# Optimization experiments

Measured on AMD Instinct MI355X. Metric: run time of the kernel, lower is better.

Reference implementation:

```python
import jax, jax.numpy as jnp
import numpy as np

T, B, C = 512, 64, 512
ALPHA = 0.6        # blend coefficient from __init__
TAU = 10.0         # LIF tau
VTH = 1.0          # LIF v_threshold (v_reset = 0, hard reset)
BN_EPS = 1e-5


def spike_fn(x):
    # forward heaviside: spike = (v - v_th >= 0)
    return (x >= 0.0).astype(x.dtype)


def setup_inputs() -> dict:
    key = jax.random.key(0)
    ks = jax.random.split(key, 7)
    x = jax.random.normal(ks[0], (T, B, C), dtype=jnp.float32)
    conv_w = jax.random.normal(ks[1], (C, C, 3), dtype=jnp.float32) / np.sqrt(3.0 * C)
    conv_b = jax.random.normal(ks[2], (C,), dtype=jnp.float32) * 0.01
    bn_gamma = 0.5 + jax.random.uniform(ks[3], (C,), dtype=jnp.float32)
    bn_beta = jax.random.normal(ks[4], (C,), dtype=jnp.float32) * 0.1
    bn_mean = jax.random.normal(ks[5], (C,), dtype=jnp.float32) * 0.1
    bn_var = 0.5 + jax.random.uniform(ks[6], (C,), dtype=jnp.float32)
    return {"x": x, "conv_w": conv_w, "conv_b": conv_b,
            "bn_gamma": bn_gamma, "bn_beta": bn_beta,
            "bn_mean": bn_mean, "bn_var": bn_var}


def reference(x, conv_w, conv_b, bn_gamma, bn_beta, bn_mean, bn_var):
    # x: (T, B, C). Conv1d(k=3, pad=1) on a length-1 sequence reduces to a
    # dense matmul with the middle kernel tap: out = prev @ w[:,:,1].T + b.
    w1 = conv_w[:, :, 1]                      # (C_out, C_in)
    inv_std = bn_gamma * jax.lax.rsqrt(bn_var + BN_EPS)   # fused BN scale
    Bsz, Csz = x.shape[1], x.shape[2]

    def step(carry, x_t):
        prev, v = carry                        # prev: (B, C), v: (B, C) membrane
        conv = jnp.einsum('bc,dc->bd', prev, w1) + conv_b
        bn = (conv - bn_mean) * inv_std + bn_beta
        # LIF (decay_input=True, v_reset=0): v += (x - v) / tau
        v = v + (bn - v) / TAU
        s = spike_fn(v - VTH)
        v = v * (1.0 - s)                      # hard reset to 0
        new = (1.0 - ALPHA) * x_t + ALPHA * s  # alpha blend
        return (new, v), new                   # prev_state detached in torch; no-op for fwd

    init = (jnp.zeros((Bsz, Csz), x.dtype), jnp.zeros((Bsz, Csz), x.dtype))
    _, out = jax.lax.scan(step, init, x)       # out: (T, B, C)
    return out
```

## Files before the change

kernel.cpp:

```cpp
#include <hip/hip_runtime.h>
#include <hip/hip_bf16.h>
#include <stdint.h>

#define T_STEPS 512
#define BATCH 64
#define CH 512

using short8 = __attribute__((ext_vector_type(8))) short;
using f32x4  = __attribute__((ext_vector_type(4))) float;

__device__ __forceinline__ unsigned short f2b(float f) {
    union { __hip_bfloat16 h; unsigned short u; } c;
    c.h = __float2bfloat16(f);
    return c.u;
}
__device__ __forceinline__ float b2f(unsigned short h) {
    union { unsigned u; float f; } c; c.u = ((unsigned)h) << 16;
    return c.f;
}

#define LDS_BARRIER() do {                                   \
    __builtin_amdgcn_sched_barrier(0);                       \
    asm volatile("s_waitcnt lgkmcnt(0)" ::: "memory");       \
    __builtin_amdgcn_s_barrier();                            \
    __builtin_amdgcn_sched_barrier(0);                       \
} while (0)

__global__ void prep(const float* __restrict__ cw, const float* __restrict__ cb,
                     const float* __restrict__ gamma, const float* __restrict__ beta,
                     const float* __restrict__ mean, const float* __restrict__ var,
                     unsigned short* __restrict__ wb,
                     float* __restrict__ wt,
                     float* __restrict__ isb,
                     float* __restrict__ k0p,
                     int* __restrict__ flag) {
    int idx = blockIdx.x * 256 + threadIdx.x;
    if (idx == 0) *flag = 0x7fffffff;
    if (idx >= CH * CH) return;
    int d = idx >> 9, c = idx & 511;
    float is = gamma[d] * rsqrtf(var[d] + 1e-5f);
    float w = cw[((size_t)d * CH + c) * 3 + 1];
    wb[idx] = f2b(0.04f * is * w);
    wt[(size_t)c * CH + d] = w;
    if (c == 0) {
        isb[d] = is;
        k0p[d] = 0.1f * ((cb[d] - mean[d]) * is + beta[d]);
    }
}

#define GBM 128
#define PADK 40

__global__ __launch_bounds__(512, 2) void gemm_fused(
    const float* __restrict__ Xp,
    const unsigned short* __restrict__ wbp,
    const float* __restrict__ k0p,
    unsigned short* __restrict__ Wbuf,
    float* __restrict__ outp,
    int Mc)
{
    __shared__ __align__(16) unsigned short As[2][GBM][PADK];
    __shared__ __align__(16) unsigned short Bs[2][512][PADK];
    int tid = threadIdx.x;
    int lane = tid & 63, wid = tid >> 6;
    int wm = wid >> 2, wn = wid & 3;
    int i0 = blockIdx.x * GBM;
    int fm = lane & 15, fq = lane >> 4;
    int kq = fq * 8;

    int ar = tid >> 2;
    int ak = (tid & 3) * 8;

    int grow = i0 + ar;
    bool arv = grow < Mc;
    int growc = arv ? grow : (Mc - 1);
    const float* xrow = &Xp[(size_t)growc * CH + ak];
    float* orow = &outp[(size_t)grow * CH + ak];
    const unsigned short* brow = &wbp[(size_t)ar * CH + ak];

    f32x4 acc[4][8] = {};

    float4 sa0[2], sa1[2];
    short8 sb[2][4];

    {
        sa0[0] = *(const float4*)&xrow[0];
        sa1[0] = *(const float4*)&xrow[4];
        #pragma unroll
        for (int p = 0; p < 4; ++p)
            sb[0][p] = *(const short8*)&brow[(size_t)p * 128 * CH];
        short8 av;
        av[0]=f2b(sa0[0].x); av[1]=f2b(sa0[0].y); av[2]=f2b(sa0[0].z); av[3]=f2b(sa0[0].w);
        av[4]=f2b(sa1[0].x); av[5]=f2b(sa1[0].y); av[6]=f2b(sa1[0].z); av[7]=f2b(sa1[0].w);
        *(short8*)&As[0][ar][ak] = av;
        #pragma unroll
        for (int p = 0; p < 4; ++p)
            *(short8*)&Bs[0][ar + p * 128][ak] = sb[0][p];
        if (arv) {
            *(float4*)&orow[0] = make_float4(0.4f*sa0[0].x, 0.4f*sa0[0].y, 0.4f*sa0[0].z, 0.4f*sa0[0].w);
            *(float4*)&orow[4] = make_float4(0.4f*sa1[0].x, 0.4f*sa1[0].y, 0.4f*sa1[0].z, 0.4f*sa1[0].w);
        }
        sa0[1] = *(const float4*)&xrow[32];
        sa1[1] = *(const float4*)&xrow[36];
        #pragma unroll
        for (int p = 0; p < 4; ++p)
            sb[1][p] = *(const short8*)&brow[(size_t)p * 128 * CH + 32];
    }
    LDS_BARRIER();

    for (int ks = 0; ks < 16; ++ks) {
        int cur = ks & 1;
        int kw = ks + 1;
        int ki = ks + 2;
        if (kw < 16) {
            int sw = kw & 1;
            short8 av;
            av[0]=f2b(sa0[sw].x); av[1]=f2b(sa0[sw].y); av[2]=f2b(sa0[sw].z); av[3]=f2b(sa0[sw].w);
            av[4]=f2b(sa1[sw].x); av[5]=f2b(sa1[sw].y); av[6]=f2b(sa1[sw].z); av[7]=f2b(sa1[sw].w);
            *(short8*)&As[cur ^ 1][ar][ak] = av;
            #pragma unroll
            for (int p = 0; p < 4; ++p)
                *(short8*)&Bs[cur ^ 1][ar + p * 128][ak] = sb[sw][p];
            if (arv) {
                *(float4*)&orow[kw * 32]     = make_float4(0.4f*sa0[sw].x, 0.4f*sa0[sw].y, 0.4f*sa0[sw].z, 0.4f*sa0[sw].w);
                *(float4*)&orow[kw * 32 + 4] = make_float4(0.4f*sa1[sw].x, 0.4f*sa1[sw].y, 0.4f*sa1[sw].z, 0.4f*sa1[sw].w);
            }
        }
        if (ki < 16) {
            int si = ki & 1;
            sa0[si] = *(const float4*)&xrow[ki * 32];
            sa1[si] = *(const float4*)&xrow[ki * 32 + 4];
            #pragma unroll
            for (int p = 0; p < 4; ++p)
                sb[si][p] = *(const short8*)&brow[(size_t)p * 128 * CH + ki * 32];
        }
        short8 af[4];
        #pragma unroll
        for (int i = 0; i < 4; ++i)
            af[i] = *(const short8*)&As[cur][wm * 64 + i * 16 + fm][kq];
        #pragma unroll
        for (int jh = 0; jh < 2; ++jh) {
            short8 bfr[4];
            #pragma unroll
            for (int j = 0; j < 4; ++j)
                bfr[j] = *(const short8*)&Bs[cur][wn * 128 + (jh * 4 + j) * 16 + fm][kq];
            #pragma unroll
            for (int i = 0; i < 4; ++i)
                #pragma unroll
                for (int j = 0; j < 4; ++j)
                    acc[i][jh * 4 + j] = __builtin_amdgcn_mfma_f32_16x16x32_bf16(af[i], bfr[j], acc[i][jh * 4 + j], 0, 0, 0);
        }
        LDS_BARRIER();
    }

    float b0e[8];
    #pragma unroll
    for (int j = 0; j < 8; ++j) b0e[j] = k0p[wn * 128 + j * 16 + fm];
    #pragma unroll
    for (int i = 0; i < 4; ++i)
        #pragma unroll
        for (int r = 0; r < 4; ++r) {
            int row = i0 + wm * 64 + i * 16 + fq * 4 + r;
            if (row < Mc) {
                #pragma unroll
                for (int j = 0; j < 8; ++j) {
                    int col = wn * 128 + j * 16 + fm;
                    Wbuf[(size_t)row * CH + col] = f2b(acc[i][j][r] + b0e[j]);
                }
            }
        }
}

__device__ __forceinline__ short8 wload(const unsigned short* Wbuf, int t, int a0, int b, int c0) {
    int r = t - 1 - a0; if (r < 0) r = 0;
    return *(const short8*)&Wbuf[((size_t)r * BATCH + b) * CH + c0];
}

__global__ __launch_bounds__(64) void scan_a(
    const unsigned short* __restrict__ Wbuf,
    const float* __restrict__ k0p,
    float* __restrict__ Sbuf,
    int t0, int a0, int segs)
{
    int b = blockIdx.x & (BATCH - 1);
    int seg = blockIdx.x >> 6;
    int lane = threadIdx.x, c0 = lane * 8;
    int tstart = t0 + seg * 64;

    float B0[8];
    #pragma unroll
    for (int k = 0; k < 8; ++k) B0[k] = k0p[c0 + k];

    float S[8] = {};
    short8 pz[8];
    #pragma unroll
    for (int p = 0; p < 8; ++p) pz[p] = wload(Wbuf, tstart + p, a0, b, c0);

    for (int ii = 0; ii < 64; ii += 8) {
        #pragma unroll
        for (int p = 0; p < 8; ++p) {
            int t = tstart + ii + p;
            short8 zv = pz[p];
            int tn = ii + p + 8;
            if (tn < 64) pz[p] = wload(Wbuf, tstart + tn, a0, b, c0);
            #pragma unroll
            for (int k = 0; k < 8; ++k) {
                float wv = (t == 0) ? B0[k] : b2f((unsigned short)zv[k]);
                S[k] = fmaf(0.9f, S[k], wv);
            }
        }
    }
    float* sp = &Sbuf[((size_t)b * segs + seg) * CH + c0];
    *(float4*)&sp[0] = make_float4(S[0], S[1], S[2], S[3]);
    *(float4*)&sp[4] = make_float4(S[4], S[5], S[6], S[7]);
}

__global__ __launch_bounds__(64) void scan_c(
    const unsigned short* __restrict__ Wbuf,
    const float* __restrict__ k0p,
    const float* __restrict__ Sbuf,
    const float* __restrict__ vcin,
    float* __restrict__ vcout,
    int* __restrict__ flag,
    int t0, int a0, int segs, int chunk_idx)
{
    const float F = 1.1790184577738595e-3f;
    int b = blockIdx.x & (BATCH - 1);
    int seg = blockIdx.x >> 6;
    int lane = threadIdx.x, c0 = lane * 8;
    int tstart = t0 + seg * 64;

    float B0[8];
    #pragma unroll
    for (int k = 0; k < 8; ++k) B0[k] = k0p[c0 + k];

    float v[8];
    if (t0 == 0) {
        #pragma unroll
        for (int k = 0; k < 8; ++k) v[k] = 0.0f;
    } else {
        const float* vp = &vcin[(size_t)b * CH + c0];
        float4 v0 = *(const float4*)&vp[0], v1 = *(const float4*)&vp[4];
        v[0]=v0.x; v[1]=v0.y; v[2]=v0.z; v[3]=v0.w; v[4]=v1.x; v[5]=v1.y; v[6]=v1.z; v[7]=v1.w;
    }
    for (int u = 0; u < seg; ++u) {
        const float* sp = &Sbuf[((size_t)b * segs + u) * CH + c0];
        float4 s0 = *(const float4*)&sp[0], s1 = *(const float4*)&sp[4];
        float sv[8] = {s0.x, s0.y, s0.z, s0.w, s1.x, s1.y, s1.z, s1.w};
        #pragma unroll
        for (int k = 0; k < 8; ++k) v[k] = fmaf(v[k], F, sv[k]);
    }

    bool anyhit = false;
    short8 pz[8];
    #pragma unroll
    for (int p = 0; p < 8; ++p) pz[p] = wload(Wbuf, tstart + p, a0, b, c0);

    for (int ii = 0; ii < 64; ii += 8) {
        #pragma unroll
        for (int p = 0; p < 8; ++p) {
            int t = tstart + ii + p;
            short8 zv = pz[p];
            int tn = ii + p + 8;
            if (tn < 64) pz[p] = wload(Wbuf, tstart + tn, a0, b, c0);
            float m = -1e30f;
            #pragma unroll
            for (int k = 0; k < 8; ++k) {
                float wv = (t == 0) ? B0[k] : b2f((unsigned short)zv[k]);
                v[k] = fmaf(0.9f, v[k], wv);
                m = fmaxf(m, v[k]);
            }
            anyhit |= (m >= 0.995f);
        }
    }
    if (__ballot(anyhit) != 0ULL && lane == 0) atomicMin(flag, chunk_idx);
    if (seg == segs - 1) {
        float* vp = &vcout[(size_t)b * CH + c0];
        *(float4*)&vp[0] = make_float4(v[0], v[1], v[2], v[3]);
        *(float4*)&vp[4] = make_float4(v[4], v[5], v[6], v[7]);
    }
}

__global__ __launch_bounds__(64) void seq_fix(
    const float* __restrict__ x,
    const float* __restrict__ wt,
    const unsigned short* __restrict__ Wbuf,
    const float* __restrict__ isb,
    const float* __restrict__ k0p,
    const int* __restrict__ flag,
    const float* __restrict__ vcin,
    float* __restrict__ out,
    float* __restrict__ v_state,
    unsigned long long* __restrict__ s_state,
    int t0, int t1, int a0, int chunk_idx, int save_state)
{
    int fl = *flag;
    if (fl > chunk_idx) return;
    int b = blockIdx.x;
    int lane = threadIdx.x;
    int c0 = lane * 8;

    float is6[8], B0[8];
    #pragma unroll
    for (int k = 0; k < 8; ++k) {
        is6[k] = 0.06f * isb[c0 + k];
        B0[k]  = k0p[c0 + k];
    }

    float v[8];
    unsigned long long mk[8];
    if (t0 == 0) {
        #pragma unroll
        for (int k = 0; k < 8; ++k) v[k] = 0.0f;
        #pragma unroll
        for (int j = 0; j < 8; ++j) mk[j] = 0ULL;
    } else if (fl == chunk_idx) {
        #pragma unroll
        for (int k = 0; k < 8; ++k) v[k] = vcin[(size_t)b * CH + c0 + k];
        #pragma unroll
        for (int j = 0; j < 8; ++j) mk[j] = 0ULL;
    } else {
        #pragma unroll
        for (int k = 0; k < 8; ++k) v[k] = v_state[(size_t)b * CH + c0 + k];
        #pragma unroll
        for (int j = 0; j < 8; ++j) mk[j] = s_state[b * 8 + j];
    }

    float xc[8]; short8 wc;
    {
        const float4* xp = (const float4*)&x[((size_t)t0 * BATCH + b) * CH + c0];
        float4 x0 = xp[0], x1 = xp[1];
        xc[0]=x0.x; xc[1]=x0.y; xc[2]=x0.z; xc[3]=x0.w; xc[4]=x1.x; xc[5]=x1.y; xc[6]=x1.z; xc[7]=x1.w;
        wc = wload(Wbuf, t0, a0, b, c0);
    }
    for (int t = t0; t < t1; ++t) {
        float xn[8]; short8 wn_;
        if (t + 1 < t1) {
            const float4* xp = (const float4*)&x[((size_t)(t + 1) * BATCH + b) * CH + c0];
            float4 x0 = xp[0], x1 = xp[1];
            xn[0]=x0.x; xn[1]=x0.y; xn[2]=x0.z; xn[3]=x0.w; xn[4]=x1.x; xn[5]=x1.y; xn[6]=x1.z; xn[7]=x1.w;
            wn_ = wload(Wbuf, t + 1, a0, b, c0);
        }
        float acc[8] = {};
        unsigned long long anym = mk[0]|mk[1]|mk[2]|mk[3]|mk[4]|mk[5]|mk[6]|mk[7];
        if (anym) {
            #pragma unroll
            for (int j = 0; j < 8; ++j) {
                unsigned long long m = mk[j];
                while (m) {
                    int l = __builtin_ctzll(m); m &= m - 1;
                    const float4* wr = (const float4*)&wt[(size_t)(l * 8 + j) * CH + c0];
                    float4 w0 = wr[0], w1 = wr[1];
                    acc[0]+=w0.x; acc[1]+=w0.y; acc[2]+=w0.z; acc[3]+=w0.w;
                    acc[4]+=w1.x; acc[5]+=w1.y; acc[6]+=w1.z; acc[7]+=w1.w;
                }
            }
        }
        bool s[8];
        #pragma unroll
        for (int k = 0; k < 8; ++k) {
            float wv = (t == 0) ? B0[k] : b2f((unsigned short)wc[k]);
            float vv = fmaf(0.9f, v[k], fmaf(is6[k], acc[k], wv));
            s[k] = (vv >= 1.0f);
            v[k] = s[k] ? 0.0f : vv;
        }
        float4* op = (float4*)&out[((size_t)t * BATCH + b) * CH + c0];
        op[0] = make_float4(fmaf(0.4f,xc[0],s[0]?0.6f:0.f), fmaf(0.4f,xc[1],s[1]?0.6f:0.f),
                            fmaf(0.4f,xc[2],s[2]?0.6f:0.f), fmaf(0.4f,xc[3],s[3]?0.6f:0.f));
        op[1] = make_float4(fmaf(0.4f,xc[4],s[4]?0.6f:0.f), fmaf(0.4f,xc[5],s[5]?0.6f:0.f),
                            fmaf(0.4f,xc[6],s[6]?0.6f:0.f), fmaf(0.4f,xc[7],s[7]?0.6f:0.f));
        #pragma unroll
        for (int j = 0; j < 8; ++j) mk[j] = __ballot(s[j]);
        #pragma unroll
        for (int k = 0; k < 8; ++k) xc[k] = xn[k];
        wc = wn_;
    }
    if (save_state) {
        #pragma unroll
        for (int k = 0; k < 8; ++k) v_state[(size_t)b * CH + c0 + k] = v[k];
        if (lane < 8) s_state[b * 8 + lane] = mk[lane];
    }
}

extern "C" void kernel_launch(void* const* d_in, const int* in_sizes, int n_in,
                              void* d_out, int out_size, void* d_ws, size_t ws_size,
                              hipStream_t stream) {
    const float* x     = (const float*)d_in[0];
    const float* cw    = (const float*)d_in[1];
    const float* cb    = (const float*)d_in[2];
    const float* gamma = (const float*)d_in[3];
    const float* beta  = (const float*)d_in[4];
    const float* mean  = (const float*)d_in[5];
    const float* var   = (const float*)d_in[6];
    float* out = (float*)d_out;

    char* ws = (char*)d_ws;
    size_t off = 0;
    auto alloc = [&](size_t bytes) -> char* {
        char* p = ws + off;
        off = (off + bytes + 255) & ~(size_t)255;
        return p;
    };
    unsigned short* wb = (unsigned short*)alloc((size_t)CH * CH * 2);
    float* wt  = (float*)alloc((size_t)CH * CH * 4);
    float* isb = (float*)alloc(CH * 4);
    float* k0p = (float*)alloc(CH * 4);
    int* flag  = (int*)alloc(256);
    float* vst = (float*)alloc((size_t)BATCH * CH * 4);
    unsigned long long* sst = (unsigned long long*)alloc(BATCH * 8 * 8);
    float* vca = (float*)alloc((size_t)BATCH * CH * 4);
    float* vcb = (float*)alloc((size_t)BATCH * CH * 4);
    float* Sb  = (float*)alloc((size_t)BATCH * 8 * CH * 4);
    unsigned short* Wbuf = (unsigned short*)(ws + off);

    size_t avail = (ws_size > off) ? ws_size - off : 0;
    long rows = (long)(avail / ((size_t)BATCH * CH * 2));
    long cs = ((rows - 1) / 64) * 64;
    if (cs > T_STEPS) cs = T_STEPS;
    if (cs < 64) cs = 64;
    int CS = (int)cs;

    hipLaunchKernelGGL(prep, dim3((CH * CH + 255) / 256), dim3(256), 0, stream,
                       cw, cb, gamma, beta, mean, var, wb, wt, isb, k0p, flag);

    float *vin = vca, *vout = vcb;
    int k = 0;
    for (int t0 = 0; t0 < T_STEPS; t0 += CS, ++k) {
        int t1 = t0 + CS; if (t1 > T_STEPS) t1 = T_STEPS;
        int a0 = (t0 == 0) ? 0 : t0 - 1;
        int gend = (t1 == T_STEPS) ? T_STEPS : t1 - 1;
        int Mc = (gend - a0) * BATCH;
        hipLaunchKernelGGL(gemm_fused, dim3((Mc + GBM - 1) / GBM), dim3(512), 0, stream,
                           x + (size_t)a0 * BATCH * CH, wb, k0p, Wbuf,
                           out + (size_t)a0 * BATCH * CH, Mc);
        int segs = (t1 - t0) / 64;
        hipLaunchKernelGGL(scan_a, dim3(BATCH * segs), dim3(64), 0, stream,
                           Wbuf, k0p, Sb, t0, a0, segs);
        hipLaunchKernelGGL(scan_c, dim3(BATCH * segs), dim3(64), 0, stream,
                           Wbuf, k0p, Sb, vin, vout, flag, t0, a0, segs, k);
        hipLaunchKernelGGL(seq_fix, dim3(BATCH), dim3(64), 0, stream,
                           x, wt, Wbuf, isb, k0p, flag, vin, out, vst, sst,
                           t0, t1, a0, k, (t1 < T_STEPS) ? 1 : 0);
        float* tmp = vin; vin = vout; vout = tmp;
    }
}
```

Before: 65.69 us.

## Retile fused GEMM to 128x256 blocks with 2D grid and K=64 steps

Splits the GEMM's N dimension across a second grid axis, so each block computes a 128x256 tile instead of the full 512 columns. K steps go from 32 to 64, with a single LDS buffer and two barriers per step instead of double-buffered LDS. Only the blockIdx.y==0 blocks write the 0.4*x output. The aim is more blocks and fewer accumulators per thread for better occupancy, at the cost of reading and converting X twice and adding a barrier per step.

```diff
diff --git a/kernel.cpp b/kernel.cpp
--- a/kernel.cpp
+++ b/kernel.cpp
@@ -49,9 +49,10 @@
 }
 
 #define GBM 128
-#define PADK 40
-
-__global__ __launch_bounds__(512, 2) void gemm_fused(
+#define GBN 256
+#define PADK2 72
+
+__global__ __launch_bounds__(512) void gemm_fused(
     const float* __restrict__ Xp,
     const unsigned short* __restrict__ wbp,
     const float* __restrict__ k0p,
@@ -59,103 +60,111 @@
     float* __restrict__ outp,
     int Mc)
 {
-    __shared__ __align__(16) unsigned short As[2][GBM][PADK];
-    __shared__ __align__(16) unsigned short Bs[2][512][PADK];
+    __shared__ __align__(16) unsigned short As[GBM][PADK2];
+    __shared__ __align__(16) unsigned short Bs[GBN][PADK2];
     int tid = threadIdx.x;
     int lane = tid & 63, wid = tid >> 6;
     int wm = wid >> 2, wn = wid & 3;
     int i0 = blockIdx.x * GBM;
+    int n0 = blockIdx.y * GBN;
+    bool wout = (blockIdx.y == 0);
     int fm = lane & 15, fq = lane >> 4;
     int kq = fq * 8;
 
-    int ar = tid >> 2;
-    int ak = (tid & 3) * 8;
+    int ar  = tid >> 2;
+    int akc = (tid & 3) * 16;
+    int br  = tid >> 1;
+    int bkc = (tid & 1) * 32;
 
     int grow = i0 + ar;
     bool arv = grow < Mc;
     int growc = arv ? grow : (Mc - 1);
-    const float* xrow = &Xp[(size_t)growc * CH + ak];
-    float* orow = &outp[(size_t)grow * CH + ak];
-    const unsigned short* brow = &wbp[(size_t)ar * CH + ak];
-
-    f32x4 acc[4][8] = {};
-
-    float4 sa0[2], sa1[2];
-    short8 sb[2][4];
-
-    {
-        sa0[0] = *(const float4*)&xrow[0];
-        sa1[0] = *(const float4*)&xrow[4];
-        #pragma unroll
-        for (int p = 0; p < 4; ++p)
-            sb[0][p] = *(const short8*)&brow[(size_t)p * 128 * CH];
+    const float* xrow = &Xp[(size_t)growc * CH + akc];
+    float* orow = &outp[(size_t)grow * CH + akc];
+    const unsigned short* brow = &wbp[(size_t)(n0 + br) * CH + bkc];
+
+    f32x4 acc[4][4] = {};
+    float4 sx[2][4];
+    short8 sbv[2][4];
+
+    #pragma unroll
+    for (int q = 0; q < 4; ++q) sx[0][q] = *(const float4*)&xrow[q * 4];
+    #pragma unroll
+    for (int q = 0; q < 4; ++q) sbv[0][q] = *(const short8*)&brow[q * 8];
+    #pragma unroll
+    for (int q = 0; q < 2; ++q) {
+        float4 a0 = sx[0][2 * q], a1 = sx[0][2 * q + 1];
         short8 av;
-        av[0]=f2b(sa0[0].x); av[1]=f2b(sa0[0].y); av[2]=f2b(sa0[0].z); av[3]=f2b(sa0[0].w);
-        av[4]=f2b(sa1[0].x); av[5]=f2b(sa1[0].y); av[6]=f2b(sa1[0].z); av[7]=f2b(sa1[0].w);
-        *(short8*)&As[0][ar][ak] = av;
-        #pragma unroll
-        for (int p = 0; p < 4; ++p)
-            *(short8*)&Bs[0][ar + p * 128][ak] = sb[0][p];
-        if (arv) {
-            *(float4*)&orow[0] = make_float4(0.4f*sa0[0].x, 0.4f*sa0[0].y, 0.4f*sa0[0].z, 0.4f*sa0[0].w);
-            *(float4*)&orow[4] = make_float4(0.4f*sa1[0].x, 0.4f*sa1[0].y, 0.4f*sa1[0].z, 0.4f*sa1[0].w);
-        }
-        sa0[1] = *(const float4*)&xrow[32];
-        sa1[1] = *(const float4*)&xrow[36];
-        #pragma unroll
-        for (int p = 0; p < 4; ++p)
-            sb[1][p] = *(const short8*)&brow[(size_t)p * 128 * CH + 32];
-    }
+        av[0]=f2b(a0.x); av[1]=f2b(a0.y); av[2]=f2b(a0.z); av[3]=f2b(a0.w);
+        av[4]=f2b(a1.x); av[5]=f2b(a1.y); av[6]=f2b(a1.z); av[7]=f2b(a1.w);
+        *(short8*)&As[ar][akc + q * 8] = av;
+    }
+    #pragma unroll
+    for (int q = 0; q < 4; ++q) *(short8*)&Bs[br][bkc + q * 8] = sbv[0][q];
+    if (wout && arv) {
+        #pragma unroll
+        for (int q = 0; q < 4; ++q) {
+            float4 a = sx[0][q];
+            *(float4*)&orow[q * 4] = make_float4(0.4f*a.x, 0.4f*a.y, 0.4f*a.z, 0.4f*a.w);
+        }
+    }
+    #pragma unroll
+    for (int q = 0; q < 4; ++q) sx[1][q] = *(const float4*)&xrow[64 + q * 4];
+    #pragma unroll
+    for (int q = 0; q < 4; ++q) sbv[1][q] = *(const short8*)&brow[64 + q * 8];
     LDS_BARRIER();
 
-    for (int ks = 0; ks < 16; ++ks) {
-        int cur = ks & 1;
-        int kw = ks + 1;
-        int ki = ks + 2;
-        if (kw < 16) {
-            int sw = kw & 1;
-            short8 av;
-            av[0]=f2b(sa0[sw].x); av[1]=f2b(sa0[sw].y); av[2]=f2b(sa0[sw].z); av[3]=f2b(sa0[sw].w);
-            av[4]=f2b(sa1[sw].x); av[5]=f2b(sa1[sw].y); av[6]=f2b(sa1[sw].z); av[7]=f2b(sa1[sw].w);
-            *(short8*)&As[cur ^ 1][ar][ak] = av;
-            #pragma unroll
-            for (int p = 0; p < 4; ++p)
-                *(short8*)&Bs[cur ^ 1][ar + p * 128][ak] = sb[sw][p];
-            if (arv) {
-                *(float4*)&orow[kw * 32]     = make_float4(0.4f*sa0[sw].x, 0.4f*sa0[sw].y, 0.4f*sa0[sw].z, 0.4f*sa0[sw].w);
-                *(float4*)&orow[kw * 32 + 4] = make_float4(0.4f*sa1[sw].x, 0.4f*sa1[sw].y, 0.4f*sa1[sw].z, 0.4f*sa1[sw].w);
-            }
-        }
-        if (ki < 16) {
-            int si = ki & 1;
-            sa0[si] = *(const float4*)&xrow[ki * 32];
-            sa1[si] = *(const float4*)&xrow[ki * 32 + 4];
-            #pragma unroll
-            for (int p = 0; p < 4; ++p)
-                sb[si][p] = *(const short8*)&brow[(size_t)p * 128 * CH + ki * 32];
-        }
-        short8 af[4];
-        #pragma unroll
-        for (int i = 0; i < 4; ++i)
-            af[i] = *(const short8*)&As[cur][wm * 64 + i * 16 + fm][kq];
-        #pragma unroll
-        for (int jh = 0; jh < 2; ++jh) {
-            short8 bfr[4];
+    #pragma unroll 2
+    for (int ks = 0; ks < 8; ++ks) {
+        #pragma unroll
+        for (int kh = 0; kh < 2; ++kh) {
+            short8 af[4], bf[4];
+            #pragma unroll
+            for (int i = 0; i < 4; ++i)
+                af[i] = *(const short8*)&As[wm * 64 + i * 16 + fm][kh * 32 + kq];
             #pragma unroll
             for (int j = 0; j < 4; ++j)
-                bfr[j] = *(const short8*)&Bs[cur][wn * 128 + (jh * 4 + j) * 16 + fm][kq];
+                bf[j] = *(const short8*)&Bs[wn * 64 + j * 16 + fm][kh * 32 + kq];
             #pragma unroll
             for (int i = 0; i < 4; ++i)
                 #pragma unroll
                 for (int j = 0; j < 4; ++j)
-                    acc[i][jh * 4 + j] = __builtin_amdgcn_mfma_f32_16x16x32_bf16(af[i], bfr[j], acc[i][jh * 4 + j], 0, 0, 0);
+                    acc[i][j] = __builtin_amdgcn_mfma_f32_16x16x32_bf16(af[i], bf[j], acc[i][j], 0, 0, 0);
+        }
+        if (ks + 2 < 8) {
+            int si = ks & 1, ko = (ks + 2) * 64;
+            #pragma unroll
+            for (int q = 0; q < 4; ++q) sx[si][q] = *(const float4*)&xrow[ko + q * 4];
+            #pragma unroll
+            for (int q = 0; q < 4; ++q) sbv[si][q] = *(const short8*)&brow[ko + q * 8];
         }
         LDS_BARRIER();
-    }
-
-    float b0e[8];
-    #pragma unroll
-    for (int j = 0; j < 8; ++j) b0e[j] = k0p[wn * 128 + j * 16 + fm];
+        if (ks + 1 < 8) {
+            int sw = (ks + 1) & 1, ko = (ks + 1) * 64;
+            #pragma unroll
+            for (int q = 0; q < 2; ++q) {
+                float4 a0 = sx[sw][2 * q], a1 = sx[sw][2 * q + 1];
+                short8 av;
+                av[0]=f2b(a0.x); av[1]=f2b(a0.y); av[2]=f2b(a0.z); av[3]=f2b(a0.w);
+                av[4]=f2b(a1.x); av[5]=f2b(a1.y); av[6]=f2b(a1.z); av[7]=f2b(a1.w);
+                *(short8*)&As[ar][akc + q * 8] = av;
+            }
+            #pragma unroll
+            for (int q = 0; q < 4; ++q) *(short8*)&Bs[br][bkc + q * 8] = sbv[sw][q];
+            if (wout && arv) {
+                #pragma unroll
+                for (int q = 0; q < 4; ++q) {
+                    float4 a = sx[sw][q];
+                    *(float4*)&orow[ko + q * 4] = make_float4(0.4f*a.x, 0.4f*a.y, 0.4f*a.z, 0.4f*a.w);
+                }
+            }
+        }
+        LDS_BARRIER();
+    }
+
+    float b0e[4];
+    #pragma unroll
+    for (int j = 0; j < 4; ++j) b0e[j] = k0p[n0 + wn * 64 + j * 16 + fm];
     #pragma unroll
     for (int i = 0; i < 4; ++i)
         #pragma unroll
@@ -163,8 +172,8 @@
             int row = i0 + wm * 64 + i * 16 + fq * 4 + r;
             if (row < Mc) {
                 #pragma unroll
-                for (int j = 0; j < 8; ++j) {
-                    int col = wn * 128 + j * 16 + fm;
+                for (int j = 0; j < 4; ++j) {
+                    int col = n0 + wn * 64 + j * 16 + fm;
                     Wbuf[(size_t)row * CH + col] = f2b(acc[i][j][r] + b0e[j]);
                 }
             }
@@ -430,7 +439,7 @@
         int a0 = (t0 == 0) ? 0 : t0 - 1;
         int gend = (t1 == T_STEPS) ? T_STEPS : t1 - 1;
         int Mc = (gend - a0) * BATCH;
-        hipLaunchKernelGGL(gemm_fused, dim3((Mc + GBM - 1) / GBM), dim3(512), 0, stream,
+        hipLaunchKernelGGL(gemm_fused, dim3((Mc + GBM - 1) / GBM, CH / GBN), dim3(512), 0, stream,
                            x + (size_t)a0 * BATCH * CH, wb, k0p, Wbuf,
                            out + (size_t)a0 * BATCH * CH, Mc);
         int segs = (t1 - t0) / 64;
```

Measured after the change: 88.19 us. +34.2%, slower.
